# Kernel optimization log

Measured on AMD Instinct MI355X. Metric: run time of the kernel, lower is better.

Reference implementation:

```python
import jax, jax.numpy as jnp
import numpy as np

EPS = 1e-8
D = 1024      # embedding_dim
NH = 4        # num_heads
HD = D // NH  # head_dim
B, S = 4, 2048


def setup_inputs() -> dict:
    key = jax.random.key(0)
    k1, k2 = jax.random.split(key)
    x = jax.random.normal(k1, (B, S, 4 * D), dtype=jnp.float32)
    # small-init std = sqrt(2/(5*head_dim)) as in reset_parameters
    std = float(np.sqrt(2.0 / (5.0 * HD)))
    gate_weights = jax.random.normal(k2, (4, NH, HD, HD), dtype=jnp.float32) * std
    # biases: z,i,o zero; f gets powerlaw init (block 0 of 1 -> exponent 0.3)
    term = jnp.arange(HD, dtype=jnp.float32) / (HD - 1.0)
    f_bias = -(-5.0 + 12.0 * term ** 0.3)  # [HD]
    gate_biases = jnp.zeros((4, NH, HD), dtype=jnp.float32)
    gate_biases = gate_biases.at[2].set(jnp.broadcast_to(f_bias, (NH, HD)))
    return {"x_gate_inputs": x, "gate_weights": gate_weights, "gate_biases": gate_biases}


def _slstm_forward(x, W, biases):
    Bn, Sn, _ = x.shape
    # split into 4 gate pre-activations and apply headwise linear per gate
    xg = x.reshape(Bn, Sn, 4, NH, HD)           # gate order z,i,f,o along axis 2
    xg = jnp.moveaxis(xg, 2, 0)                  # [4,B,S,NH,HD]
    # headwise projection: einsum over head-in dim, per gate g and head h
    gates = jnp.einsum('gbshi,ghoi->gbsho', xg, W) + biases[:, None, None]  # [4,B,S,NH,HD]
    gates = jnp.moveaxis(gates, 2, 0)            # [S,4,B,NH,HD] for scan over time

    h0 = jnp.zeros((Bn, NH, HD), dtype=x.dtype)
    carry0 = (h0, h0, h0, jnp.zeros((Bn, NH, HD), dtype=jnp.float32))

    def step(carry, g_t):
        h, c, n, m = carry
        z_b, i_b, f_b, o_b = g_t[0], g_t[1], g_t[2], g_t[3]
        z_val = jnp.tanh(z_b)
        o_val = jax.nn.sigmoid(o_b)
        # faithful to original: exp then log(.+EPS), in m-state dtype (fp32)
        log_f = jnp.log(jnp.exp(f_b).astype(jnp.float32) + EPS)
        log_i = jnp.log(jnp.exp(i_b).astype(jnp.float32) + EPS)
        m_new = jnp.maximum(log_f + m, log_i)
        i_hat = jnp.exp(log_i - m_new).astype(x.dtype)
        f_hat = jnp.exp(log_f + m - m_new).astype(x.dtype)
        c_new = f_hat * c + i_hat * z_val
        n_new = f_hat * n + i_hat
        h_new = o_val * (c_new / (n_new + EPS))
        return (h_new, c_new, n_new, m_new), h_new

    (h_f, c_f, n_f, m_f), hs = jax.lax.scan(step, carry0, gates)
    h_seq = jnp.moveaxis(hs, 0, 1)               # [B,S,NH,HD]
    return h_seq, (h_f, c_f, n_f, m_f)


def reference(x_gate_inputs, gate_weights, gate_biases):
    h_seq, (h_f, c_f, n_f, m_f) = _slstm_forward(x_gate_inputs, gate_weights, gate_biases)
    return h_seq, h_f, c_f, n_f, m_f
```

## Files before the change

### kernel.cpp

```cpp
#include <hip/hip_runtime.h>
#include <cstdint>

#define S_LEN   2048
#define BATCH   4
#define NCH     4096
#define PLANE   ((size_t)S_LEN * NCH)
#define CHUNK   32
#define NCHUNK  64
#define SN      ((size_t)NCHUNK * NCH)
#define EPS     1e-8f

using bf16x8 = __attribute__((ext_vector_type(8))) short;
using f32x4  = __attribute__((ext_vector_type(4))) float;
typedef unsigned short u16;

__device__ __forceinline__ short f2bf(float f) {
  uint32_t u = __builtin_bit_cast(uint32_t, f);
  u += 0x7fffu + ((u >> 16) & 1u);
  return (short)(u >> 16);
}
__device__ __forceinline__ float bf2f(u16 u) {
  return __builtin_bit_cast(float, (uint32_t)u << 16);
}
__device__ __forceinline__ void lds_barrier() {
  asm volatile("s_waitcnt lgkmcnt(0)\n\ts_barrier" ::: "memory");
}

__global__ __launch_bounds__(1024) void gates_gemm4(
    const float* __restrict__ x, const float* __restrict__ W,
    const float* __restrict__ bias,
    u16* __restrict__ gz16, float* __restrict__ gi, float* __restrict__ gf,
    u16* __restrict__ go16) {
  __shared__ u16 As[2][16 * 272];

  const int gh  = blockIdx.x;
  const int rg  = blockIdx.y;
  const int g   = gh >> 2, hh = gh & 3;
  const int tid = threadIdx.x;
  const int wave = tid >> 6, lane = tid & 63;
  const int l16 = lane & 15, quad = lane >> 4;
  const int n0  = wave * 16;
  const int row0 = rg * 256;

  bf16x8 Bf[8];
  {
    const float* wp = W + ((size_t)gh << 16) + (n0 + l16) * 256 + quad * 8;
#pragma unroll
    for (int kt = 0; kt < 8; ++kt) {
      float4 w0 = *(const float4*)(wp + kt * 32);
      float4 w1 = *(const float4*)(wp + kt * 32 + 4);
      bf16x8 b;
      b[0] = f2bf(w0.x); b[1] = f2bf(w0.y); b[2] = f2bf(w0.z); b[3] = f2bf(w0.w);
      b[4] = f2bf(w1.x); b[5] = f2bf(w1.y); b[6] = f2bf(w1.z); b[7] = f2bf(w1.w);
      Bf[kt] = b;
    }
  }
  const float bv = bias[gh * 256 + n0 + l16];

  const int sr = tid >> 6, sc = tid & 63;
  const float* sbase = x + (size_t)(row0 + sr) * 4096 + g * 1024 + hh * 256 + sc * 4;

  auto swrite = [&](int buf, float4 v) {
    ushort4 u;
    u.x = (u16)f2bf(v.x); u.y = (u16)f2bf(v.y);
    u.z = (u16)f2bf(v.z); u.w = (u16)f2bf(v.w);
    *(ushort4*)&As[buf][sr * 272 + sc * 4] = u;
  };

  float4 pf[2];
  pf[0] = *(const float4*)(sbase);
  pf[1] = *(const float4*)(sbase + (size_t)16 * 4096);
  swrite(0, pf[0]);
  lds_barrier();

  f32x4 acc[16];
#pragma unroll
  for (int t = 0; t < 16; ++t) acc[t] = (f32x4){0.f, 0.f, 0.f, 0.f};

#pragma unroll
  for (int t = 0; t < 16; ++t) {
    if (t + 2 < 16) pf[t & 1] = *(const float4*)(sbase + (size_t)(t + 2) * 16 * 4096);

#pragma unroll
    for (int kt = 0; kt < 8; ++kt) {
      bf16x8 a = *(const bf16x8*)&As[t & 1][l16 * 272 + kt * 32 + quad * 8];
      acc[t] = __builtin_amdgcn_mfma_f32_16x16x32_bf16(a, Bf[kt], acc[t], 0, 0, 0);
    }

    if (t + 1 < 16) {
      swrite((t + 1) & 1, pf[(t + 1) & 1]);
      lds_barrier();
    }
  }

#pragma unroll
  for (int t = 0; t < 16; ++t) {
#pragma unroll
    for (int rr = 0; rr < 4; ++rr) {
      int rowi = row0 + t * 16 + quad * 4 + rr;
      int sx = rowi & (S_LEN - 1);
      int bx = rowi >> 11;
      size_t idx = (size_t)sx * NCH + bx * 1024 + hh * 256 + n0 + l16;
      float v = acc[t][rr] + bv;
      if (g == 1)      gi[idx] = v;
      else if (g == 2) gf[idx] = v;
      else if (g == 0) {
        float tz = 1.f - 2.f * __builtin_amdgcn_rcpf(1.f + __expf(2.f * v));
        gz16[idx] = (u16)f2bf(tz);
      } else {
        float s = __builtin_amdgcn_rcpf(1.f + __expf(-v));
        go16[idx] = (u16)f2bf(s);
      }
    }
  }
}

__global__ __launch_bounds__(256, 4) void scan_pass1(
    const u16* __restrict__ gz16, const float* __restrict__ gi,
    const float* __restrict__ gf, float* __restrict__ sums) {
  const int t  = blockIdx.x * 256 + threadIdx.x;
  const int ch = t & (NCH - 1);
  const int ck = t >> 12;
  const size_t base = (size_t)ck * CHUNK * NCH + ch;

  float A = 0.f, Bv = -1e30f, D = 0.f, Dn = 0.f;

  u16 zb[3][8]; float ib[3][8], fb[3][8];

  auto loadg = [&](int buf, int grp) {
#pragma unroll
    for (int j = 0; j < 8; ++j) {
      size_t off = base + (size_t)(grp * 8 + j) * NCH;
      zb[buf][j] = gz16[off]; ib[buf][j] = gi[off]; fb[buf][j] = gf[off];
    }
  };

  loadg(0, 0);
  loadg(1, 1);

#pragma unroll
  for (int grp = 0; grp < 4; ++grp) {
    if (grp + 2 < 4) loadg((grp + 2) % 3, grp + 2);
    const int b = grp % 3;
#pragma unroll
    for (int j = 0; j < 8; ++j) {
      float z = bf2f(zb[b][j]), i = ib[b][j], f = fb[b][j];
      float Bn = fmaxf(Bv + f, i);
      float e1 = __expf(Bv + f - Bn);
      float e2 = __expf(i - Bn);
      D  = e1 * D + e2 * z;
      Dn = e1 * Dn + e2;
      A += f;
      Bv = Bn;
    }
  }

  const size_t idx = (size_t)ck * NCH + ch;
  sums[idx]          = A;
  sums[SN + idx]     = Bv;
  sums[2 * SN + idx] = D;
  sums[3 * SN + idx] = Dn;
}

__global__ __launch_bounds__(256) void scan_pass2(
    const float* __restrict__ sums, float* __restrict__ ent) {
  const int gt   = blockIdx.x * 256 + threadIdx.x;
  const int ch   = gt >> 6;
  const int lane = threadIdx.x & 63;

  const size_t idx = (size_t)lane * NCH + ch;
  float A = sums[idx], B = sums[SN + idx];
  float D = sums[2 * SN + idx], N = sums[3 * SN + idx];

#pragma unroll
  for (int d = 1; d < 64; d <<= 1) {
    float A1 = __shfl_up(A, d, 64);
    float B1 = __shfl_up(B, d, 64);
    float D1 = __shfl_up(D, d, 64);
    float N1 = __shfl_up(N, d, 64);
    if (lane >= d) {
      float Bn = fmaxf(B1 + A, B);
      float s1 = __expf(B1 + A - Bn);
      float s2 = __expf(B - Bn);
      D = s1 * D1 + s2 * D;
      N = s1 * N1 + s2 * N;
      B = Bn;
      A = A1 + A;
    }
  }

  float Ax = __shfl_up(A, 1, 64), Bx = __shfl_up(B, 1, 64);
  float Dx = __shfl_up(D, 1, 64), Nx = __shfl_up(N, 1, 64);
  if (lane == 0) { Ax = 0.f; Bx = -1e30f; Dx = 0.f; Nx = 0.f; }

  float mE = fmaxf(Ax, Bx);
  float sc = __expf(Bx - mE);
  ent[idx]          = sc * Dx;
  ent[SN + idx]     = sc * Nx;
  ent[2 * SN + idx] = mE;
}

__global__ __launch_bounds__(256, 4) void scan_pass3(
    const u16* __restrict__ gz16, const float* __restrict__ gi,
    const float* __restrict__ gf, const u16* __restrict__ go16,
    const float* __restrict__ ent, float* __restrict__ out) {
  const int t  = blockIdx.x * 256 + threadIdx.x;
  const int ch = t & (NCH - 1);
  const int ck = t >> 12;

  const size_t idx0 = (size_t)ck * NCH + ch;
  float c = ent[idx0];
  float n = ent[SN + idx0];
  float m = ent[2 * SN + idx0];

  const int b = ch >> 10, d = ch & 1023;
  const size_t base = (size_t)ck * CHUNK * NCH + ch;
  float* hout = out + (size_t)b * (S_LEN * 1024) + (size_t)(ck * CHUNK) * 1024 + d;

  u16 zb[3][8], ob[3][8]; float ib[3][8], fb[3][8];

  auto loadg = [&](int buf, int grp) {
#pragma unroll
    for (int j = 0; j < 8; ++j) {
      size_t off = base + (size_t)(grp * 8 + j) * NCH;
      zb[buf][j] = gz16[off]; ib[buf][j] = gi[off];
      fb[buf][j] = gf[off];   ob[buf][j] = go16[off];
    }
  };

  loadg(0, 0);
  loadg(1, 1);

  float hv = 0.f;
#pragma unroll
  for (int grp = 0; grp < 4; ++grp) {
    if (grp + 2 < 4) loadg((grp + 2) % 3, grp + 2);
    const int bu = grp % 3;
#pragma unroll
    for (int j = 0; j < 8; ++j) {
      float z = bf2f(zb[bu][j]), i = ib[bu][j], f = fb[bu][j], o = bf2f(ob[bu][j]);
      float mn = fmaxf(f + m, i);
      float fh = __expf(f + m - mn);
      float ih = __expf(i - mn);
      c = fh * c + ih * z;
      n = fh * n + ih;
      m = mn;
      hv = o * c * __builtin_amdgcn_rcpf(n + EPS);
      hout[(size_t)(grp * 8 + j) * 1024] = hv;
    }
  }

  if (ck == NCHUNK - 1) {
    float* fin = out + (size_t)BATCH * S_LEN * 1024;
    fin[ch]            = hv;
    fin[NCH + ch]      = c;
    fin[2 * NCH + ch]  = n;
    fin[3 * NCH + ch]  = m;
  }
}

extern "C" void kernel_launch(void* const* d_in, const int* in_sizes, int n_in,
                              void* d_out, int out_size, void* d_ws, size_t ws_size,
                              hipStream_t stream) {
  const float* x    = (const float*)d_in[0];
  const float* W    = (const float*)d_in[1];
  const float* bias = (const float*)d_in[2];
  float* out = (float*)d_out;

  u16*   gz16 = (u16*)d_ws;
  float* gi   = (float*)(gz16 + PLANE);
  float* gf   = gi + PLANE;
  u16*   go16 = (u16*)(gf + PLANE);
  float* sums = (float*)(go16 + PLANE);
  float* ent  = sums + 4 * SN;

  gates_gemm4<<<dim3(16, 32), dim3(1024), 0, stream>>>(x, W, bias, gz16, gi, gf, go16);
  scan_pass1<<<dim3(1024), dim3(256), 0, stream>>>(gz16, gi, gf, sums);
  scan_pass2<<<dim3(1024), dim3(256), 0, stream>>>(sums, ent);
  scan_pass3<<<dim3(1024), dim3(256), 0, stream>>>(gz16, gi, gf, go16, ent, out);
}
```

Baseline: 279.5 us.

## Transpose gate buffers to channel-major and fuse scan passes one and two

The GEMM now writes gate pre-activations in channel-major (time-contiguous) layout, storing each tile as vector writes right after its MFMA chain instead of holding all accumulators. The chunk-summary pass is merged into the cross-chunk prefix kernel, which saves a launch and the round trip through the sums buffer. The final pass reads each chunk's gates with contiguous vector loads. The cost is that in the scan kernels a single thread's vector load covers a contiguous time run, so neighbouring lanes are strided by 2048 elements. Coalescing across a wave may be worse than in the old layout, where lanes read adjacent channels.

```diff
diff --git a/kernel.cpp b/kernel.cpp
--- a/kernel.cpp
+++ b/kernel.cpp
@@ -26,11 +26,11 @@
   asm volatile("s_waitcnt lgkmcnt(0)\n\ts_barrier" ::: "memory");
 }
 
-__global__ __launch_bounds__(1024) void gates_gemm4(
+__global__ __launch_bounds__(1024) void gates_gemm5(
     const float* __restrict__ x, const float* __restrict__ W,
     const float* __restrict__ bias,
-    u16* __restrict__ gz16, float* __restrict__ gi, float* __restrict__ gf,
-    u16* __restrict__ go16) {
+    u16* __restrict__ zT, float* __restrict__ iT, float* __restrict__ fT,
+    u16* __restrict__ oT) {
   __shared__ u16 As[2][16 * 272];
 
   const int gh  = blockIdx.x;
@@ -67,24 +67,49 @@
     *(ushort4*)&As[buf][sr * 272 + sc * 4] = u;
   };
 
+  const int bb = row0 >> 11;
+  const size_t ch = (size_t)bb * 1024 + hh * 256 + n0 + l16;
+  const int sbase0 = (row0 & (S_LEN - 1)) + quad * 4;
+
   float4 pf[2];
   pf[0] = *(const float4*)(sbase);
   pf[1] = *(const float4*)(sbase + (size_t)16 * 4096);
   swrite(0, pf[0]);
   lds_barrier();
 
-  f32x4 acc[16];
-#pragma unroll
-  for (int t = 0; t < 16; ++t) acc[t] = (f32x4){0.f, 0.f, 0.f, 0.f};
-
 #pragma unroll
   for (int t = 0; t < 16; ++t) {
     if (t + 2 < 16) pf[t & 1] = *(const float4*)(sbase + (size_t)(t + 2) * 16 * 4096);
 
+    f32x4 acc = (f32x4){0.f, 0.f, 0.f, 0.f};
 #pragma unroll
     for (int kt = 0; kt < 8; ++kt) {
       bf16x8 a = *(const bf16x8*)&As[t & 1][l16 * 272 + kt * 32 + quad * 8];
-      acc[t] = __builtin_amdgcn_mfma_f32_16x16x32_bf16(a, Bf[kt], acc[t], 0, 0, 0);
+      acc = __builtin_amdgcn_mfma_f32_16x16x32_bf16(a, Bf[kt], acc, 0, 0, 0);
+    }
+
+    {
+      const size_t off = ch * S_LEN + (size_t)(sbase0 + t * 16);
+      float v0 = acc[0] + bv, v1 = acc[1] + bv, v2 = acc[2] + bv, v3 = acc[3] + bv;
+      if (g == 1) {
+        *(float4*)&iT[off] = make_float4(v0, v1, v2, v3);
+      } else if (g == 2) {
+        *(float4*)&fT[off] = make_float4(v0, v1, v2, v3);
+      } else if (g == 0) {
+        ushort4 u;
+        u.x = (u16)f2bf(1.f - 2.f * __builtin_amdgcn_rcpf(1.f + __expf(2.f * v0)));
+        u.y = (u16)f2bf(1.f - 2.f * __builtin_amdgcn_rcpf(1.f + __expf(2.f * v1)));
+        u.z = (u16)f2bf(1.f - 2.f * __builtin_amdgcn_rcpf(1.f + __expf(2.f * v2)));
+        u.w = (u16)f2bf(1.f - 2.f * __builtin_amdgcn_rcpf(1.f + __expf(2.f * v3)));
+        *(ushort4*)&zT[off] = u;
+      } else {
+        ushort4 u;
+        u.x = (u16)f2bf(__builtin_amdgcn_rcpf(1.f + __expf(-v0)));
+        u.y = (u16)f2bf(__builtin_amdgcn_rcpf(1.f + __expf(-v1)));
+        u.z = (u16)f2bf(__builtin_amdgcn_rcpf(1.f + __expf(-v2)));
+        u.w = (u16)f2bf(__builtin_amdgcn_rcpf(1.f + __expf(-v3)));
+        *(ushort4*)&oT[off] = u;
+      }
     }
 
     if (t + 1 < 16) {
@@ -92,85 +117,39 @@
       lds_barrier();
     }
   }
-
-#pragma unroll
-  for (int t = 0; t < 16; ++t) {
-#pragma unroll
-    for (int rr = 0; rr < 4; ++rr) {
-      int rowi = row0 + t * 16 + quad * 4 + rr;
-      int sx = rowi & (S_LEN - 1);
-      int bx = rowi >> 11;
-      size_t idx = (size_t)sx * NCH + bx * 1024 + hh * 256 + n0 + l16;
-      float v = acc[t][rr] + bv;
-      if (g == 1)      gi[idx] = v;
-      else if (g == 2) gf[idx] = v;
-      else if (g == 0) {
-        float tz = 1.f - 2.f * __builtin_amdgcn_rcpf(1.f + __expf(2.f * v));
-        gz16[idx] = (u16)f2bf(tz);
-      } else {
-        float s = __builtin_amdgcn_rcpf(1.f + __expf(-v));
-        go16[idx] = (u16)f2bf(s);
-      }
-    }
-  }
-}
-
-__global__ __launch_bounds__(256, 4) void scan_pass1(
-    const u16* __restrict__ gz16, const float* __restrict__ gi,
-    const float* __restrict__ gf, float* __restrict__ sums) {
-  const int t  = blockIdx.x * 256 + threadIdx.x;
-  const int ch = t & (NCH - 1);
-  const int ck = t >> 12;
-  const size_t base = (size_t)ck * CHUNK * NCH + ch;
-
-  float A = 0.f, Bv = -1e30f, D = 0.f, Dn = 0.f;
-
-  u16 zb[3][8]; float ib[3][8], fb[3][8];
-
-  auto loadg = [&](int buf, int grp) {
-#pragma unroll
-    for (int j = 0; j < 8; ++j) {
-      size_t off = base + (size_t)(grp * 8 + j) * NCH;
-      zb[buf][j] = gz16[off]; ib[buf][j] = gi[off]; fb[buf][j] = gf[off];
-    }
-  };
-
-  loadg(0, 0);
-  loadg(1, 1);
-
-#pragma unroll
-  for (int grp = 0; grp < 4; ++grp) {
-    if (grp + 2 < 4) loadg((grp + 2) % 3, grp + 2);
-    const int b = grp % 3;
-#pragma unroll
-    for (int j = 0; j < 8; ++j) {
-      float z = bf2f(zb[b][j]), i = ib[b][j], f = fb[b][j];
-      float Bn = fmaxf(Bv + f, i);
-      float e1 = __expf(Bv + f - Bn);
-      float e2 = __expf(i - Bn);
-      D  = e1 * D + e2 * z;
-      Dn = e1 * Dn + e2;
-      A += f;
-      Bv = Bn;
-    }
-  }
-
-  const size_t idx = (size_t)ck * NCH + ch;
-  sums[idx]          = A;
-  sums[SN + idx]     = Bv;
-  sums[2 * SN + idx] = D;
-  sums[3 * SN + idx] = Dn;
-}
-
-__global__ __launch_bounds__(256) void scan_pass2(
-    const float* __restrict__ sums, float* __restrict__ ent) {
+}
+
+__global__ __launch_bounds__(256, 4) void scan_pass12(
+    const u16* __restrict__ zT, const float* __restrict__ iT,
+    const float* __restrict__ fT, float* __restrict__ ent) {
   const int gt   = blockIdx.x * 256 + threadIdx.x;
   const int ch   = gt >> 6;
   const int lane = threadIdx.x & 63;
-
-  const size_t idx = (size_t)lane * NCH + ch;
-  float A = sums[idx], B = sums[SN + idx];
-  float D = sums[2 * SN + idx], N = sums[3 * SN + idx];
+  const size_t base = (size_t)ch * S_LEN + (size_t)lane * CHUNK;
+
+  float4  iv[8], fv[8];
+  ushort4 zv[8];
+#pragma unroll
+  for (int j = 0; j < 8; ++j) iv[j] = *(const float4*)&iT[base + j * 4];
+#pragma unroll
+  for (int j = 0; j < 8; ++j) fv[j] = *(const float4*)&fT[base + j * 4];
+#pragma unroll
+  for (int j = 0; j < 8; ++j) zv[j] = *(const ushort4*)&zT[base + j * 4];
+
+  float A = 0.f, B = -1e30f, D = 0.f, N = 0.f;
+#pragma unroll
+  for (int s = 0; s < 32; ++s) {
+    float i = ((const float*)&iv[s >> 2])[s & 3];
+    float f = ((const float*)&fv[s >> 2])[s & 3];
+    float z = bf2f(((const u16*)&zv[s >> 2])[s & 3]);
+    float Bn = fmaxf(B + f, i);
+    float e1 = __expf(B + f - Bn);
+    float e2 = __expf(i - Bn);
+    D = e1 * D + e2 * z;
+    N = e1 * N + e2;
+    A += f;
+    B = Bn;
+  }
 
 #pragma unroll
   for (int d = 1; d < 64; d <<= 1) {
@@ -195,14 +174,15 @@
 
   float mE = fmaxf(Ax, Bx);
   float sc = __expf(Bx - mE);
+  const size_t idx = (size_t)lane * NCH + ch;
   ent[idx]          = sc * Dx;
   ent[SN + idx]     = sc * Nx;
   ent[2 * SN + idx] = mE;
 }
 
 __global__ __launch_bounds__(256, 4) void scan_pass3(
-    const u16* __restrict__ gz16, const float* __restrict__ gi,
-    const float* __restrict__ gf, const u16* __restrict__ go16,
+    const u16* __restrict__ zT, const float* __restrict__ iT,
+    const float* __restrict__ fT, const u16* __restrict__ oT,
     const float* __restrict__ ent, float* __restrict__ out) {
   const int t  = blockIdx.x * 256 + threadIdx.x;
   const int ch = t & (NCH - 1);
@@ -213,41 +193,36 @@
   float n = ent[SN + idx0];
   float m = ent[2 * SN + idx0];
 
+  const size_t base = (size_t)ch * S_LEN + (size_t)ck * CHUNK;
+  float4  iv[8], fv[8];
+  ushort4 zv[8], ov[8];
+#pragma unroll
+  for (int j = 0; j < 8; ++j) iv[j] = *(const float4*)&iT[base + j * 4];
+#pragma unroll
+  for (int j = 0; j < 8; ++j) fv[j] = *(const float4*)&fT[base + j * 4];
+#pragma unroll
+  for (int j = 0; j < 8; ++j) zv[j] = *(const ushort4*)&zT[base + j * 4];
+#pragma unroll
+  for (int j = 0; j < 8; ++j) ov[j] = *(const ushort4*)&oT[base + j * 4];
+
   const int b = ch >> 10, d = ch & 1023;
-  const size_t base = (size_t)ck * CHUNK * NCH + ch;
   float* hout = out + (size_t)b * (S_LEN * 1024) + (size_t)(ck * CHUNK) * 1024 + d;
 
-  u16 zb[3][8], ob[3][8]; float ib[3][8], fb[3][8];
-
-  auto loadg = [&](int buf, int grp) {
-#pragma unroll
-    for (int j = 0; j < 8; ++j) {
-      size_t off = base + (size_t)(grp * 8 + j) * NCH;
-      zb[buf][j] = gz16[off]; ib[buf][j] = gi[off];
-      fb[buf][j] = gf[off];   ob[buf][j] = go16[off];
-    }
-  };
-
-  loadg(0, 0);
-  loadg(1, 1);
-
   float hv = 0.f;
 #pragma unroll
-  for (int grp = 0; grp < 4; ++grp) {
-    if (grp + 2 < 4) loadg((grp + 2) % 3, grp + 2);
-    const int bu = grp % 3;
-#pragma unroll
-    for (int j = 0; j < 8; ++j) {
-      float z = bf2f(zb[bu][j]), i = ib[bu][j], f = fb[bu][j], o = bf2f(ob[bu][j]);
-      float mn = fmaxf(f + m, i);
-      float fh = __expf(f + m - mn);
-      float ih = __expf(i - mn);
-      c = fh * c + ih * z;
-      n = fh * n + ih;
-      m = mn;
-      hv = o * c * __builtin_amdgcn_rcpf(n + EPS);
-      hout[(size_t)(grp * 8 + j) * 1024] = hv;
-    }
+  for (int s = 0; s < 32; ++s) {
+    float i = ((const float*)&iv[s >> 2])[s & 3];
+    float f = ((const float*)&fv[s >> 2])[s & 3];
+    float z = bf2f(((const u16*)&zv[s >> 2])[s & 3]);
+    float o = bf2f(((const u16*)&ov[s >> 2])[s & 3]);
+    float mn = fmaxf(f + m, i);
+    float fh = __expf(f + m - mn);
+    float ih = __expf(i - mn);
+    c = fh * c + ih * z;
+    n = fh * n + ih;
+    m = mn;
+    hv = o * c * __builtin_amdgcn_rcpf(n + EPS);
+    hout[(size_t)s * 1024] = hv;
   }
 
   if (ck == NCHUNK - 1) {
@@ -267,15 +242,13 @@
   const float* bias = (const float*)d_in[2];
   float* out = (float*)d_out;
 
-  u16*   gz16 = (u16*)d_ws;
-  float* gi   = (float*)(gz16 + PLANE);
-  float* gf   = gi + PLANE;
-  u16*   go16 = (u16*)(gf + PLANE);
-  float* sums = (float*)(go16 + PLANE);
-  float* ent  = sums + 4 * SN;
-
-  gates_gemm4<<<dim3(16, 32), dim3(1024), 0, stream>>>(x, W, bias, gz16, gi, gf, go16);
-  scan_pass1<<<dim3(1024), dim3(256), 0, stream>>>(gz16, gi, gf, sums);
-  scan_pass2<<<dim3(1024), dim3(256), 0, stream>>>(sums, ent);
-  scan_pass3<<<dim3(1024), dim3(256), 0, stream>>>(gz16, gi, gf, go16, ent, out);
-}
+  u16*   zT  = (u16*)d_ws;
+  float* iT  = (float*)(zT + PLANE);
+  float* fT  = iT + PLANE;
+  u16*   oT  = (u16*)(fT + PLANE);
+  float* ent = (float*)(oT + PLANE);
+
+  gates_gemm5<<<dim3(16, 32), dim3(1024), 0, stream>>>(x, W, bias, zT, iT, fT, oT);
+  scan_pass12<<<dim3(1024), dim3(256), 0, stream>>>(zT, iT, fT, ent);
+  scan_pass3<<<dim3(1024), dim3(256), 0, stream>>>(zT, iT, fT, oT, ent, out);
+}
```

After: 328.7 us. 17.6% more time.
